# Optimization experiments

Hardware: AMD Instinct MI355X
Metric: run time of the kernel (lower is better)

The kernel has to match this reference:

```python
import jax, jax.numpy as jnp
import numpy as np

B, N, F_IN, H, C = 32768, 12, 128, 4, 64  # batch, nodes/graph, input_dim, heads, hidden_dim
NEG_SLOPE = 0.2  # PyG GATConv default leaky_relu slope


def setup_inputs() -> dict:
    key = jax.random.key(0)
    ks = jax.random.split(key, 16)
    def xavier(k, shape):
        fan_in, fan_out = shape[0], int(np.prod(shape[1:]))
        lim = float(np.sqrt(6.0 / (fan_in + fan_out)))
        return jax.random.uniform(k, shape, jnp.float32, -lim, lim)
    return {
        "node_features": jax.random.normal(ks[0], (B, N, F_IN), jnp.float32),
        "W1": xavier(ks[1], (F_IN, H, C)),
        "a_src1": xavier(ks[2], (H, C)),
        "a_dst1": xavier(ks[3], (H, C)),
        "b1": jnp.zeros((H * C,), jnp.float32),
        "W2": xavier(ks[4], (H * C, 1, C)),
        "a_src2": xavier(ks[5], (1, C)),
        "a_dst2": xavier(ks[6], (1, C)),
        "b2": jnp.zeros((C,), jnp.float32),
        # classifier head: 64 -> 32 -> 1
        "Wc1": xavier(ks[7], (C, C // 2)),
        "bc1": jnp.zeros((C // 2,), jnp.float32),
        "Wc2": xavier(ks[8], (C // 2, 1)),
        "bc2": jnp.zeros((1,), jnp.float32),
    }


def gat_dense(x, W, a_src, a_dst, bias, concat):
    # x: [B, N, F].  Fully-connected graph + self-loops (PyG GATConv default)
    # == dense attention over all N nodes of each graph.
    h = jnp.einsum("bnf,fhc->bnhc", x, W)               # [B,N,H,C]
    e_src = jnp.einsum("bnhc,hc->bnh", h, a_src)         # alpha contrib of source j
    e_dst = jnp.einsum("bnhc,hc->bnh", h, a_dst)         # alpha contrib of target i
    # edge (j -> i): logit = leaky_relu(e_dst[i] + e_src[j])
    logits = jax.nn.leaky_relu(e_dst[:, :, None, :] + e_src[:, None, :, :], NEG_SLOPE)  # [B,i,j,H]
    alpha = jax.nn.softmax(logits, axis=2)               # softmax over neighbors j
    out = jnp.einsum("bijh,bjhc->bihc", alpha, h)        # aggregate
    if concat:
        out = out.reshape(out.shape[0], out.shape[1], -1)
    else:
        out = out.mean(axis=2)
    return out + bias


def reference(node_features, W1, a_src1, a_dst1, b1, W2, a_src2, a_dst2, b2,
              Wc1, bc1, Wc2, bc2):
    # eval mode: dropouts are identity; is_finetune=False so finetune_block skipped
    x = jax.nn.elu(gat_dense(node_features, W1, a_src1, a_dst1, b1, concat=True))   # [B,N,256]
    x = jax.nn.elu(gat_dense(x, W2, a_src2, a_dst2, b2, concat=False))              # [B,N,64]
    g = x.mean(axis=1)                                                              # global_mean_pool -> [B,64]
    hdn = jax.nn.relu(g @ Wc1 + bc1)
    logits = hdn @ Wc2 + bc2                                                        # [B,1]
    return logits
```

## Files before the change

kernel.cpp:

```cpp
#include <hip/hip_runtime.h>
#include <math.h>

typedef __attribute__((ext_vector_type(8))) short bf16x8;
typedef __attribute__((ext_vector_type(4))) float f32x4;

namespace {
constexpr int NN  = 12;
constexpr int FIN = 128;
constexpr int D1  = 256;
constexpr int C2  = 64;
constexpr float SLOPE = 0.2f;

__device__ __forceinline__ unsigned short f2bf(float f) {
    unsigned u = __builtin_bit_cast(unsigned, f);
    u += 0x7FFFu + ((u >> 16) & 1u);
    return (unsigned short)(u >> 16);
}
__device__ __forceinline__ float elu1(float x) { return x > 0.f ? x : __expf(x) - 1.f; }
__device__ __forceinline__ float lrelu(float x) { return x > 0.f ? x : SLOPE * x; }
}

__global__ void prep_weights(const float* __restrict__ W1, const float* __restrict__ as1,
                             const float* __restrict__ ad1,
                             const float* __restrict__ W2, const float* __restrict__ as2,
                             const float* __restrict__ ad2,
                             unsigned short* __restrict__ wsB1, unsigned short* __restrict__ wsB2) {
    int t = blockIdx.x * 256 + threadIdx.x;
    if (t < 34816) {
        int i = t & 7, l = (t >> 3) & 63, kn = t >> 9;
        int kt = kn / 17, nt = kn % 17;
        int k = kt * 32 + (l >> 4) * 8 + i;
        float v = 0.f;
        if (nt < 16) {
            v = W1[k * 256 + nt * 16 + (l & 15)];
        } else {
            int cc = l & 15;
            if (cc < 4)      for (int c = 0; c < 64; ++c) v += W1[k * 256 + cc * 64 + c] * as1[cc * 64 + c];
            else if (cc < 8) for (int c = 0; c < 64; ++c) v += W1[k * 256 + (cc - 4) * 64 + c] * ad1[(cc - 4) * 64 + c];
        }
        wsB1[t] = f2bf(v);
    } else if (t < 55296) {
        int t2 = t - 34816;
        int i = t2 & 7, l = (t2 >> 3) & 63, kn = t2 >> 9;
        int kt = kn / 5, nt = kn % 5;
        int k = kt * 32 + (l >> 4) * 8 + i;
        float v = 0.f;
        if (nt < 4) {
            v = W2[k * 64 + nt * 16 + (l & 15)];
        } else {
            int cc = l & 15;
            if (cc == 0)      for (int c = 0; c < 64; ++c) v += W2[k * 64 + c] * as2[c];
            else if (cc == 1) for (int c = 0; c < 64; ++c) v += W2[k * 64 + c] * ad2[c];
        }
        wsB2[t2] = f2bf(v);
    }
}

__global__ __launch_bounds__(512, 4) void gat_mfma6(
    const float* __restrict__ x_in,
    const unsigned short* __restrict__ wsB1,
    const unsigned short* __restrict__ wsB2,
    const float* __restrict__ b1, const float* __restrict__ b2,
    const float* __restrict__ Wc1, const float* __restrict__ bc1,
    const float* __restrict__ Wc2, const float* __restrict__ bc2,
    float* __restrict__ out)
{
    __shared__ __align__(16) unsigned char R0[13056];
    __shared__ __align__(16) unsigned char R1[32768];
    __shared__ __align__(16) unsigned char R2[24576];
    __shared__ float eS1[48][4], eD1[48][4];
    __shared__ float eS2[48], eD2[48];
    __shared__ float gpool[4][64];

    const int b = blockIdx.x, t = threadIdx.x;
    const int w = t >> 6, l = t & 63, l15 = l & 15, lq = l >> 4;

    {
        const float4* xs = (const float4*)(x_in + (size_t)b * (4 * NN * FIN));
        #pragma unroll
        for (int it = 0; it < 3; ++it) {
            int q = t + 512 * it;
            float4 v = xs[q];
            int e0 = q << 2, r = e0 >> 7, k = e0 & 127;
            int addr = ((r << 8) + (k << 1)) ^ ((r & 7) << 4);
            unsigned p0 = (unsigned)f2bf(v.x) | ((unsigned)f2bf(v.y) << 16);
            unsigned p1 = (unsigned)f2bf(v.z) | ((unsigned)f2bf(v.w) << 16);
            *(uint2*)(R0 + addr) = make_uint2(p0, p1);
        }
        #pragma unroll
        for (int it = 0; it < 3; ++it)
            *(uint4*)(R2 + ((it * 512 + t) << 4)) = make_uint4(0, 0, 0, 0);
        {
            int col = t >> 1, bs = 6 + (t & 1);
            int addr = ((col << 7) + (bs << 4)) ^ ((col & 7) << 4);
            *(uint4*)(R1 + addr) = make_uint4(0, 0, 0, 0);
        }
    }
    __syncthreads();

    {
        const uint4* pb = (const uint4*)wsB1;
        const int h = w >> 1, half = w & 1;
        bf16x8 Bf[2][4];
        #pragma unroll
        for (int ngl = 0; ngl < 2; ++ngl)
            #pragma unroll
            for (int kt = 0; kt < 4; ++kt)
                Bf[ngl][kt] = __builtin_bit_cast(bf16x8, pb[(kt * 17 + (h * 4 + half * 2 + ngl)) * 64 + l]);
        bf16x8 Bfe[4];
        if (w == 0) {
            #pragma unroll
            for (int kt = 0; kt < 4; ++kt)
                Bfe[kt] = __builtin_bit_cast(bf16x8, pb[(kt * 17 + 16) * 64 + l]);
        }
        #pragma unroll
        for (int m = 0; m < 3; ++m) {
            int r = m * 16 + l15, abase = (r << 8) + (lq << 4), swz = (r & 7) << 4;
            bf16x8 Af[4];
            #pragma unroll
            for (int kt = 0; kt < 4; ++kt)
                Af[kt] = *(const bf16x8*)(R0 + ((abase + (kt << 6)) ^ swz));
            f32x4 acc[2];
            #pragma unroll
            for (int ngl = 0; ngl < 2; ++ngl) acc[ngl] = (f32x4){0.f, 0.f, 0.f, 0.f};
            #pragma unroll
            for (int ngl = 0; ngl < 2; ++ngl)
                #pragma unroll
                for (int kt = 0; kt < 4; ++kt)
                    acc[ngl] = __builtin_amdgcn_mfma_f32_16x16x32_bf16(Af[kt], Bf[ngl][kt], acc[ngl], 0, 0, 0);
            int row0 = m * 16 + lq * 4;
            #pragma unroll
            for (int ngl = 0; ngl < 2; ++ngl) {
                int col = h * 64 + (half * 2 + ngl) * 16 + l15;
                unsigned q0 = (unsigned)f2bf(acc[ngl][0]) | ((unsigned)f2bf(acc[ngl][1]) << 16);
                unsigned q1 = (unsigned)f2bf(acc[ngl][2]) | ((unsigned)f2bf(acc[ngl][3]) << 16);
                int addr = ((col << 7) + (row0 << 1)) ^ ((col & 7) << 4);
                *(uint2*)(R1 + addr) = make_uint2(q0, q1);
            }
            if (w == 0) {
                f32x4 acce = (f32x4){0.f, 0.f, 0.f, 0.f};
                #pragma unroll
                for (int kt = 0; kt < 4; ++kt)
                    acce = __builtin_amdgcn_mfma_f32_16x16x32_bf16(Af[kt], Bfe[kt], acce, 0, 0, 0);
                if (l15 < 8) {
                    #pragma unroll
                    for (int reg = 0; reg < 4; ++reg) {
                        int row = row0 + reg;
                        if (l15 < 4) eS1[row][l15] = acce[reg];
                        else         eD1[row][l15 - 4] = acce[reg];
                    }
                }
            }
        }
    }
    __syncthreads();

    if (t < 192) {
        int g = t / 48, rem = t % 48, i = rem >> 2, h = rem & 3;
        int rowi = g * 12 + i;
        float edi = eD1[rowi][h];
        float lv[12]; float mx = -1e30f;
        #pragma unroll
        for (int j = 0; j < 12; ++j) {
            float v = lrelu(edi + eS1[g * 12 + j][h]);
            lv[j] = v; mx = fmaxf(mx, v);
        }
        float s = 0.f;
        #pragma unroll
        for (int j = 0; j < 12; ++j) { lv[j] = __expf(lv[j] - mx); s += lv[j]; }
        float inv = 1.f / s;
        unsigned char* base = R2 + h * 6144;
        int rb = rowi << 7, swz = (rowi & 7) << 4, ob = g * 24;
        #pragma unroll
        for (int p = 0; p < 3; ++p) {
            unsigned q0 = (unsigned)f2bf(lv[4*p]   * inv) | ((unsigned)f2bf(lv[4*p+1] * inv) << 16);
            unsigned q1 = (unsigned)f2bf(lv[4*p+2] * inv) | ((unsigned)f2bf(lv[4*p+3] * inv) << 16);
            int addr = (rb + ob + p * 8) ^ swz;
            *(uint2*)(base + addr) = make_uint2(q0, q1);
        }
    }
    __syncthreads();

    {
        const int h = w >> 1, half = w & 1;
        bf16x8 Bh[2][2];
        #pragma unroll
        for (int kt = 0; kt < 2; ++kt)
            #pragma unroll
            for (int ntl = 0; ntl < 2; ++ntl) {
                int col = h * 64 + (half * 2 + ntl) * 16 + l15;
                int addr = ((col << 7) + (kt << 6) + (lq << 4)) ^ ((col & 7) << 4);
                Bh[kt][ntl] = *(const bf16x8*)(R1 + addr);
            }
        float b1v[2];
        #pragma unroll
        for (int ntl = 0; ntl < 2; ++ntl) b1v[ntl] = b1[h * 64 + (half * 2 + ntl) * 16 + l15];
        unsigned char* aab = R2 + h * 6144;
        bf16x8 Aa[3][2];
        #pragma unroll
        for (int m = 0; m < 3; ++m) {
            int r = m * 16 + l15, swz = (r & 7) << 4;
            #pragma unroll
            for (int kt = 0; kt < 2; ++kt)
                Aa[m][kt] = *(const bf16x8*)(aab + (((r << 7) + (kt << 6) + (lq << 4)) ^ swz));
        }
        __syncthreads();
        #pragma unroll
        for (int m = 0; m < 3; ++m) {
            #pragma unroll
            for (int ntl = 0; ntl < 2; ++ntl) {
                f32x4 acc = (f32x4){0.f, 0.f, 0.f, 0.f};
                #pragma unroll
                for (int kt = 0; kt < 2; ++kt)
                    acc = __builtin_amdgcn_mfma_f32_16x16x32_bf16(Aa[m][kt], Bh[kt][ntl], acc, 0, 0, 0);
                #pragma unroll
                for (int reg = 0; reg < 4; ++reg) {
                    int row = m * 16 + lq * 4 + reg;
                    float val = elu1(acc[reg] + b1v[ntl]);
                    int addr = ((row << 7) + (((half * 2 + ntl) * 16 + l15) << 1)) ^ ((row & 7) << 4);
                    *(unsigned short*)(aab + addr) = f2bf(val);
                }
            }
        }
    }
    __syncthreads();

    {
        if (t < 128) {
            int col = t >> 1, bs = 6 + (t & 1);
            int addr = ((col << 7) + (bs << 4)) ^ ((col & 7) << 4);
            *(uint4*)(R1 + addr) = make_uint4(0, 0, 0, 0);
        }
        if (t < 192) {
            *(uint4*)(R1 + 8192 + (t << 4)) = make_uint4(0, 0, 0, 0);
            *(uint4*)(R1 + 8192 + ((t + 192) << 4)) = make_uint4(0, 0, 0, 0);
        }
        const uint4* pb2 = (const uint4*)wsB2;
        #pragma unroll
        for (int ui = 0; ui < 2; ++ui) {
            int u = w * 2 + ui;
            if (u < 15) {
                int tile = u / 3, m = u % 3;
                bf16x8 Bg[8];
                #pragma unroll
                for (int kt = 0; kt < 8; ++kt)
                    Bg[kt] = __builtin_bit_cast(bf16x8, pb2[(kt * 5 + tile) * 64 + l]);
                int r = m * 16 + l15, swz = (r & 7) << 4;
                f32x4 acc = (f32x4){0.f, 0.f, 0.f, 0.f};
                #pragma unroll
                for (int kt = 0; kt < 8; ++kt) {
                    int addr = (kt >> 1) * 6144 + (((r << 7) + ((kt & 1) << 6) + (lq << 4)) ^ swz);
                    bf16x8 Ax = *(const bf16x8*)(R2 + addr);
                    acc = __builtin_amdgcn_mfma_f32_16x16x32_bf16(Ax, Bg[kt], acc, 0, 0, 0);
                }
                int row0 = m * 16 + lq * 4;
                if (tile < 4) {
                    int col = tile * 16 + l15;
                    unsigned q0 = (unsigned)f2bf(acc[0]) | ((unsigned)f2bf(acc[1]) << 16);
                    unsigned q1 = (unsigned)f2bf(acc[2]) | ((unsigned)f2bf(acc[3]) << 16);
                    int addr = ((col << 7) + (row0 << 1)) ^ ((col & 7) << 4);
                    *(uint2*)(R1 + addr) = make_uint2(q0, q1);
                } else if (l15 < 2) {
                    #pragma unroll
                    for (int reg = 0; reg < 4; ++reg) {
                        int row = row0 + reg;
                        if (l15 == 0) eS2[row] = acc[reg];
                        else          eD2[row] = acc[reg];
                    }
                }
            }
        }
    }
    __syncthreads();

    if (t < 48) {
        int g = t / 12;
        float edi = eD2[t];
        float lv[12]; float mx = -1e30f;
        #pragma unroll
        for (int j = 0; j < 12; ++j) {
            float v = lrelu(edi + eS2[g * 12 + j]);
            lv[j] = v; mx = fmaxf(mx, v);
        }
        float s = 0.f;
        #pragma unroll
        for (int j = 0; j < 12; ++j) { lv[j] = __expf(lv[j] - mx); s += lv[j]; }
        float inv = 1.f / s;
        int rb = t << 7, swz = (t & 7) << 4, ob = g * 24;
        #pragma unroll
        for (int p = 0; p < 3; ++p) {
            unsigned q0 = (unsigned)f2bf(lv[4*p]   * inv) | ((unsigned)f2bf(lv[4*p+1] * inv) << 16);
            unsigned q1 = (unsigned)f2bf(lv[4*p+2] * inv) | ((unsigned)f2bf(lv[4*p+3] * inv) << 16);
            int addr = 8192 + ((rb + ob + p * 8) ^ swz);
            *(uint2*)(R1 + addr) = make_uint2(q0, q1);
        }
    }
    __syncthreads();

    {
        const int otile = w & 3;
        bf16x8 Bh2[2];
        int col = otile * 16 + l15;
        #pragma unroll
        for (int kt = 0; kt < 2; ++kt) {
            int addr = ((col << 7) + (kt << 6) + (lq << 4)) ^ ((col & 7) << 4);
            Bh2[kt] = *(const bf16x8*)(R1 + addr);
        }
        float b2v = b2[col];
        const int m0 = (w < 4) ? 0 : 2, mcount = (w < 4) ? 2 : 1;
        for (int mi = 0; mi < mcount; ++mi) {
            int m = m0 + mi;
            int r = m * 16 + l15, swz = (r & 7) << 4;
            f32x4 acc = (f32x4){0.f, 0.f, 0.f, 0.f};
            #pragma unroll
            for (int kt = 0; kt < 2; ++kt) {
                bf16x8 Aa = *(const bf16x8*)(R1 + 8192 + (((r << 7) + (kt << 6) + (lq << 4)) ^ swz));
                acc = __builtin_amdgcn_mfma_f32_16x16x32_bf16(Aa, Bh2[kt], acc, 0, 0, 0);
            }
            #pragma unroll
            for (int reg = 0; reg < 4; ++reg) {
                int row = m * 16 + lq * 4 + reg;
                *(float*)(R0 + row * 272 + (col << 2)) = elu1(acc[reg] + b2v);
            }
        }
    }
    __syncthreads();

    if (t < 256) {
        int o = t & 63, g = t >> 6;
        float s = 0.f;
        #pragma unroll
        for (int j = 0; j < 12; ++j)
            s += *(const float*)(R0 + (g * 12 + j) * 272 + (o << 2));
        gpool[g][o] = s * (1.0f / 12.0f);
    }
    __syncthreads();

    if (t < 128) {
        int g = t >> 5, nr = t & 31;
        float acc = bc1[nr];
        #pragma unroll
        for (int cc = 0; cc < 64; ++cc)
            acc = fmaf(gpool[g][cc], Wc1[cc * 32 + nr], acc);
        float val = fmaxf(acc, 0.f) * Wc2[nr];
        #pragma unroll
        for (int msk = 1; msk < 32; msk <<= 1) val += __shfl_xor(val, msk);
        if (nr == 0) out[b * 4 + g] = val + bc2[0];
    }
}

__global__ __launch_bounds__(256, 4) void gat_fused_f32(
    const float* __restrict__ x_in, const float* __restrict__ W1,
    const float* __restrict__ a_src1, const float* __restrict__ a_dst1,
    const float* __restrict__ b1, const float* __restrict__ W2,
    const float* __restrict__ a_src2, const float* __restrict__ a_dst2,
    const float* __restrict__ b2, const float* __restrict__ Wc1,
    const float* __restrict__ bc1, const float* __restrict__ Wc2,
    const float* __restrict__ bc2, float* __restrict__ out)
{
    __shared__ union {
        float x_l[NN][FIN];
        struct { float h2[NN][C2]; float x3[NN][C2]; } s2;
    } u;
    __shared__ float h1s[NN][D1];
    __shared__ float x2s[NN][D1];
    __shared__ float alpha1[NN][NN][4];
    __shared__ float e_s1[NN][4], e_d1[NN][4];
    __shared__ float e_s2[NN], e_d2[NN];
    __shared__ float alpha2[NN][NN];
    __shared__ float gph[C2];
    __shared__ float hdn[32];

    const int b = blockIdx.x, t = threadIdx.x;
    const float* xb = x_in + (size_t)b * (NN * FIN);
    for (int i = t; i < NN * FIN; i += 256) (&u.x_l[0][0])[i] = xb[i];
    __syncthreads();
    {
        const int o0 = (t & 127) * 2, n0 = (t >> 7) * 6;
        float acc[6][2];
        #pragma unroll
        for (int i = 0; i < 6; ++i) { acc[i][0] = 0.f; acc[i][1] = 0.f; }
        for (int f = 0; f < FIN; f += 4) {
            float4 xv[6];
            #pragma unroll
            for (int i = 0; i < 6; ++i) xv[i] = *(const float4*)&u.x_l[n0 + i][f];
            #pragma unroll
            for (int k = 0; k < 4; ++k) {
                const float2 wv = *(const float2*)&W1[(f + k) * D1 + o0];
                #pragma unroll
                for (int i = 0; i < 6; ++i) {
                    const float xs = ((const float*)&xv[i])[k];
                    acc[i][0] = fmaf(xs, wv.x, acc[i][0]);
                    acc[i][1] = fmaf(xs, wv.y, acc[i][1]);
                }
            }
        }
        #pragma unroll
        for (int i = 0; i < 6; ++i) { h1s[n0+i][o0] = acc[i][0]; h1s[n0+i][o0+1] = acc[i][1]; }
    }
    __syncthreads();
    if (t < NN * 4) {
        const int n = t >> 2, h = t & 3;
        float es = 0.f, ed = 0.f;
        for (int c = 0; c < 64; ++c) {
            const float v = h1s[n][h * 64 + c];
            es = fmaf(v, a_src1[h * 64 + c], es);
            ed = fmaf(v, a_dst1[h * 64 + c], ed);
        }
        e_s1[n][h] = es; e_d1[n][h] = ed;
    }
    __syncthreads();
    if (t < NN * 4) {
        const int i = t >> 2, h = t & 3;
        const float edi = e_d1[i][h];
        float lv[NN]; float m = -1e30f;
        #pragma unroll
        for (int j = 0; j < NN; ++j) {
            float v = edi + e_s1[j][h]; v = v > 0.f ? v : SLOPE * v;
            lv[j] = v; m = fmaxf(m, v);
        }
        float s = 0.f;
        #pragma unroll
        for (int j = 0; j < NN; ++j) { lv[j] = __expf(lv[j] - m); s += lv[j]; }
        const float inv = 1.f / s;
        #pragma unroll
        for (int j = 0; j < NN; ++j) alpha1[i][j][h] = lv[j] * inv;
    }
    __syncthreads();
    {
        const int o = t, h = o >> 6;
        const float bo = b1[o];
        float v[NN];
        #pragma unroll
        for (int j = 0; j < NN; ++j) v[j] = h1s[j][o];
        #pragma unroll
        for (int i = 0; i < NN; ++i) {
            float acc = 0.f;
            #pragma unroll
            for (int j = 0; j < NN; ++j) acc = fmaf(alpha1[i][j][h], v[j], acc);
            x2s[i][o] = acc + bo > 0.f ? acc + bo : expm1f(acc + bo);
        }
    }
    __syncthreads();
    {
        const int c = t & 63, n0 = (t >> 6) * 3;
        float acc[3] = {0.f, 0.f, 0.f};
        for (int f = 0; f < D1; f += 4) {
            float4 xv[3];
            #pragma unroll
            for (int i = 0; i < 3; ++i) xv[i] = *(const float4*)&x2s[n0 + i][f];
            #pragma unroll
            for (int k = 0; k < 4; ++k) {
                const float wv = W2[(f + k) * C2 + c];
                #pragma unroll
                for (int i = 0; i < 3; ++i) acc[i] = fmaf(((const float*)&xv[i])[k], wv, acc[i]);
            }
        }
        #pragma unroll
        for (int i = 0; i < 3; ++i) u.s2.h2[n0 + i][c] = acc[i];
    }
    __syncthreads();
    if (t < NN) {
        float es = 0.f, ed = 0.f;
        for (int c = 0; c < 64; c += 4) {
            const float4 v  = *(const float4*)&u.s2.h2[t][c];
            const float4 as = *(const float4*)&a_src2[c];
            const float4 ad = *(const float4*)&a_dst2[c];
            es += v.x*as.x + v.y*as.y + v.z*as.z + v.w*as.w;
            ed += v.x*ad.x + v.y*ad.y + v.z*ad.z + v.w*ad.w;
        }
        e_s2[t] = es; e_d2[t] = ed;
    }
    __syncthreads();
    if (t < NN) {
        const float edi = e_d2[t];
        float lv[NN]; float m = -1e30f;
        #pragma unroll
        for (int j = 0; j < NN; ++j) {
            float v = edi + e_s2[j]; v = v > 0.f ? v : SLOPE * v;
            lv[j] = v; m = fmaxf(m, v);
        }
        float s = 0.f;
        #pragma unroll
        for (int j = 0; j < NN; ++j) { lv[j] = __expf(lv[j] - m); s += lv[j]; }
        const float inv = 1.f / s;
        #pragma unroll
        for (int j = 0; j < NN; ++j) alpha2[t][j] = lv[j] * inv;
    }
    __syncthreads();
    {
        const int c = t & 63, i0 = (t >> 6) * 3;
        float v[NN];
        #pragma unroll
        for (int j = 0; j < NN; ++j) v[j] = u.s2.h2[j][c];
        const float bc = b2[c];
        #pragma unroll
        for (int ii = 0; ii < 3; ++ii) {
            const int i = i0 + ii;
            float acc = 0.f;
            #pragma unroll
            for (int j = 0; j < NN; ++j) acc = fmaf(alpha2[i][j], v[j], acc);
            u.s2.x3[i][c] = acc + bc > 0.f ? acc + bc : expm1f(acc + bc);
        }
    }
    __syncthreads();
    if (t < C2) {
        float s = 0.f;
        #pragma unroll
        for (int i = 0; i < NN; ++i) s += u.s2.x3[i][t];
        gph[t] = s * (1.0f / NN);
    }
    __syncthreads();
    if (t < 32) {
        float acc = bc1[t];
        for (int c = 0; c < C2; ++c) acc = fmaf(gph[c], Wc1[c * 32 + t], acc);
        hdn[t] = fmaxf(acc, 0.f);
    }
    __syncthreads();
    if (t == 0) {
        float acc = bc2[0];
        #pragma unroll
        for (int k = 0; k < 32; ++k) acc = fmaf(hdn[k], Wc2[k], acc);
        out[b] = acc;
    }
}

extern "C" void kernel_launch(void* const* d_in, const int* in_sizes, int n_in,
                              void* d_out, int out_size, void* d_ws, size_t ws_size,
                              hipStream_t stream) {
    const float* x   = (const float*)d_in[0];
    const float* W1  = (const float*)d_in[1];
    const float* as1 = (const float*)d_in[2];
    const float* ad1 = (const float*)d_in[3];
    const float* b1  = (const float*)d_in[4];
    const float* W2  = (const float*)d_in[5];
    const float* as2 = (const float*)d_in[6];
    const float* ad2 = (const float*)d_in[7];
    const float* b2  = (const float*)d_in[8];
    const float* Wc1 = (const float*)d_in[9];
    const float* bc1 = (const float*)d_in[10];
    const float* Wc2 = (const float*)d_in[11];
    const float* bc2 = (const float*)d_in[12];
    float* out = (float*)d_out;

    const int B = in_sizes[0] / (NN * FIN);

    if (ws_size >= 110592 && (B % 4) == 0) {
        unsigned short* wsB1 = (unsigned short*)d_ws;
        unsigned short* wsB2 = wsB1 + 34816;
        prep_weights<<<216, 256, 0, stream>>>(W1, as1, ad1, W2, as2, ad2, wsB1, wsB2);
        gat_mfma6<<<B / 4, 512, 0, stream>>>(x, wsB1, wsB2, b1, b2, Wc1, bc1, Wc2, bc2, out);
    } else {
        gat_fused_f32<<<B, 256, 0, stream>>>(x, W1, as1, ad1, b1, W2, as2, ad2, b2,
                                             Wc1, bc1, Wc2, bc2, out);
    }
}
```

Baseline: 155.8 us.

## Swap MFMA operand roles in aggregation GEMMs for packed, contiguous LDS stores

The layer-1 and layer-2 aggregation MFMAs are transposed: features become the M dimension and nodes the N dimension. Each lane's accumulator then holds four consecutive output features, so results are written as packed 8-byte bf16 stores (or float4 bias loads) instead of scattered 2-byte stores. The layer-1 output moves to a row-major 512-byte-stride layout, which the layer-2 projection now reads with a simpler address. Layer-2 output is stored transposed with a 200-byte stride so the mean pool can read contiguous float2 pairs. This is meant to cut LDS store instruction count and bank conflicts, at the cost of new swizzle and stride patterns that could add conflicts elsewhere.

```diff
diff --git a/kernel.cpp b/kernel.cpp
--- a/kernel.cpp
+++ b/kernel.cpp
@@ -56,7 +56,7 @@
     }
 }
 
-__global__ __launch_bounds__(512, 4) void gat_mfma6(
+__global__ __launch_bounds__(512, 4) void gat_mfma7(
     const float* __restrict__ x_in,
     const unsigned short* __restrict__ wsB1,
     const unsigned short* __restrict__ wsB2,
@@ -183,43 +183,40 @@
 
     {
         const int h = w >> 1, half = w & 1;
-        bf16x8 Bh[2][2];
-        #pragma unroll
-        for (int kt = 0; kt < 2; ++kt)
-            #pragma unroll
-            for (int ntl = 0; ntl < 2; ++ntl) {
-                int col = h * 64 + (half * 2 + ntl) * 16 + l15;
-                int addr = ((col << 7) + (kt << 6) + (lq << 4)) ^ ((col & 7) << 4);
-                Bh[kt][ntl] = *(const bf16x8*)(R1 + addr);
-            }
-        float b1v[2];
-        #pragma unroll
-        for (int ntl = 0; ntl < 2; ++ntl) b1v[ntl] = b1[h * 64 + (half * 2 + ntl) * 16 + l15];
-        unsigned char* aab = R2 + h * 6144;
-        bf16x8 Aa[3][2];
-        #pragma unroll
-        for (int m = 0; m < 3; ++m) {
-            int r = m * 16 + l15, swz = (r & 7) << 4;
+        bf16x8 Ba[3][2];
+        const unsigned char* ab = R2 + h * 6144;
+        #pragma unroll
+        for (int nt = 0; nt < 3; ++nt)
+            #pragma unroll
+            for (int kt = 0; kt < 2; ++kt) {
+                int i = nt * 16 + l15;
+                Ba[nt][kt] = *(const bf16x8*)(ab + (((i << 7) + (kt << 6) + (lq << 4)) ^ ((i & 7) << 4)));
+            }
+        __syncthreads();
+        #pragma unroll
+        for (int mtl = 0; mtl < 2; ++mtl) {
+            int mt = half * 2 + mtl;
+            int o = h * 64 + mt * 16 + l15;
+            bf16x8 Ah[2];
             #pragma unroll
             for (int kt = 0; kt < 2; ++kt)
-                Aa[m][kt] = *(const bf16x8*)(aab + (((r << 7) + (kt << 6) + (lq << 4)) ^ swz));
-        }
-        __syncthreads();
-        #pragma unroll
-        for (int m = 0; m < 3; ++m) {
-            #pragma unroll
-            for (int ntl = 0; ntl < 2; ++ntl) {
+                Ah[kt] = *(const bf16x8*)(R1 + (((o << 7) + (kt << 6) + (lq << 4)) ^ ((o & 7) << 4)));
+            int o0 = h * 64 + mt * 16 + (lq << 2);
+            float4 b1v = *(const float4*)(b1 + o0);
+            float bb[4] = {b1v.x, b1v.y, b1v.z, b1v.w};
+            #pragma unroll
+            for (int nt = 0; nt < 3; ++nt) {
                 f32x4 acc = (f32x4){0.f, 0.f, 0.f, 0.f};
                 #pragma unroll
                 for (int kt = 0; kt < 2; ++kt)
-                    acc = __builtin_amdgcn_mfma_f32_16x16x32_bf16(Aa[m][kt], Bh[kt][ntl], acc, 0, 0, 0);
-                #pragma unroll
-                for (int reg = 0; reg < 4; ++reg) {
-                    int row = m * 16 + lq * 4 + reg;
-                    float val = elu1(acc[reg] + b1v[ntl]);
-                    int addr = ((row << 7) + (((half * 2 + ntl) * 16 + l15) << 1)) ^ ((row & 7) << 4);
-                    *(unsigned short*)(aab + addr) = f2bf(val);
-                }
+                    acc = __builtin_amdgcn_mfma_f32_16x16x32_bf16(Ah[kt], Ba[nt][kt], acc, 0, 0, 0);
+                float e0 = elu1(acc[0] + bb[0]), e1 = elu1(acc[1] + bb[1]);
+                float e2 = elu1(acc[2] + bb[2]), e3 = elu1(acc[3] + bb[3]);
+                int i = nt * 16 + l15;
+                unsigned q0 = (unsigned)f2bf(e0) | ((unsigned)f2bf(e1) << 16);
+                unsigned q1 = (unsigned)f2bf(e2) | ((unsigned)f2bf(e3) << 16);
+                int addr = ((i << 9) + (o0 << 1)) ^ ((i & 7) << 4);
+                *(uint2*)(R2 + addr) = make_uint2(q0, q1);
             }
         }
     }
@@ -249,7 +246,7 @@
                 f32x4 acc = (f32x4){0.f, 0.f, 0.f, 0.f};
                 #pragma unroll
                 for (int kt = 0; kt < 8; ++kt) {
-                    int addr = (kt >> 1) * 6144 + (((r << 7) + ((kt & 1) << 6) + (lq << 4)) ^ swz);
+                    int addr = ((r << 9) + (kt << 6) + (lq << 4)) ^ swz;
                     bf16x8 Ax = *(const bf16x8*)(R2 + addr);
                     acc = __builtin_amdgcn_mfma_f32_16x16x32_bf16(Ax, Bg[kt], acc, 0, 0, 0);
                 }
@@ -298,40 +295,44 @@
     __syncthreads();
 
     {
-        const int otile = w & 3;
-        bf16x8 Bh2[2];
-        int col = otile * 16 + l15;
-        #pragma unroll
-        for (int kt = 0; kt < 2; ++kt) {
-            int addr = ((col << 7) + (kt << 6) + (lq << 4)) ^ ((col & 7) << 4);
-            Bh2[kt] = *(const bf16x8*)(R1 + addr);
-        }
-        float b2v = b2[col];
-        const int m0 = (w < 4) ? 0 : 2, mcount = (w < 4) ? 2 : 1;
-        for (int mi = 0; mi < mcount; ++mi) {
-            int m = m0 + mi;
-            int r = m * 16 + l15, swz = (r & 7) << 4;
+        const int mt = w & 3;
+        const int nt0 = (w < 4) ? 0 : 2;
+        const int ntc = (w < 4) ? 2 : 1;
+        int o = mt * 16 + l15;
+        bf16x8 Ah2[2];
+        #pragma unroll
+        for (int kt = 0; kt < 2; ++kt)
+            Ah2[kt] = *(const bf16x8*)(R1 + (((o << 7) + (kt << 6) + (lq << 4)) ^ ((o & 7) << 4)));
+        int ost = mt * 16 + (lq << 2);
+        float4 b2v = *(const float4*)(b2 + ost);
+        float bb[4] = {b2v.x, b2v.y, b2v.z, b2v.w};
+        for (int ni = 0; ni < ntc; ++ni) {
+            int nt = nt0 + ni;
+            int i = nt * 16 + l15;
+            bf16x8 Ba2[2];
+            #pragma unroll
+            for (int kt = 0; kt < 2; ++kt)
+                Ba2[kt] = *(const bf16x8*)(R1 + 8192 + (((i << 7) + (kt << 6) + (lq << 4)) ^ ((i & 7) << 4)));
             f32x4 acc = (f32x4){0.f, 0.f, 0.f, 0.f};
             #pragma unroll
-            for (int kt = 0; kt < 2; ++kt) {
-                bf16x8 Aa = *(const bf16x8*)(R1 + 8192 + (((r << 7) + (kt << 6) + (lq << 4)) ^ swz));
-                acc = __builtin_amdgcn_mfma_f32_16x16x32_bf16(Aa, Bh2[kt], acc, 0, 0, 0);
-            }
-            #pragma unroll
-            for (int reg = 0; reg < 4; ++reg) {
-                int row = m * 16 + lq * 4 + reg;
-                *(float*)(R0 + row * 272 + (col << 2)) = elu1(acc[reg] + b2v);
-            }
+            for (int kt = 0; kt < 2; ++kt)
+                acc = __builtin_amdgcn_mfma_f32_16x16x32_bf16(Ah2[kt], Ba2[kt], acc, 0, 0, 0);
+            #pragma unroll
+            for (int reg = 0; reg < 4; ++reg)
+                *(float*)(R0 + (ost + reg) * 200 + (i << 2)) = elu1(acc[reg] + bb[reg]);
         }
     }
     __syncthreads();
 
     if (t < 256) {
         int o = t & 63, g = t >> 6;
+        const unsigned char* row = R0 + o * 200 + g * 48;
         float s = 0.f;
         #pragma unroll
-        for (int j = 0; j < 12; ++j)
-            s += *(const float*)(R0 + (g * 12 + j) * 272 + (o << 2));
+        for (int p = 0; p < 6; ++p) {
+            float2 v = *(const float2*)(row + p * 8);
+            s += v.x + v.y;
+        }
         gpool[g][o] = s * (1.0f / 12.0f);
     }
     __syncthreads();
@@ -549,7 +550,7 @@
         unsigned short* wsB1 = (unsigned short*)d_ws;
         unsigned short* wsB2 = wsB1 + 34816;
         prep_weights<<<216, 256, 0, stream>>>(W1, as1, ad1, W2, as2, ad2, wsB1, wsB2);
-        gat_mfma6<<<B / 4, 512, 0, stream>>>(x, wsB1, wsB2, b1, b2, Wc1, bc1, Wc2, bc2, out);
+        gat_mfma7<<<B / 4, 512, 0, stream>>>(x, wsB1, wsB2, b1, b2, Wc1, bc1, Wc2, bc2, out);
     } else {
         gat_fused_f32<<<B, 256, 0, stream>>>(x, W1, as1, ad1, b1, W2, as2, ad2, b2,
                                              Wc1, bc1, Wc2, bc2, out);
```

After: 156.2 us. No clear change (+0.2%).
